# Kernel optimization log

Hardware: AMD Instinct MI355X
Metric: run time of the kernel (lower is better)

The kernel has to match this reference:

```python
import jax, jax.numpy as jnp
import numpy as np

B, S, D, H, DK = 32, 1024, 256, 8, 32
MASK_VALUE = -1e-30  # note: NOT -inf; masked scores become ~0 pre-softmax, faithful to source


def setup_inputs() -> dict:
    key = jax.random.key(0)
    ks = jax.random.split(key, 7)
    query = jax.random.normal(ks[0], (B, S, D), dtype=jnp.float32)
    key_t = jax.random.normal(ks[1], (B, S, D), dtype=jnp.float32)
    value = jax.random.normal(ks[2], (B, S, D), dtype=jnp.float32)
    # binary observation mask over key positions
    mask = (jax.random.uniform(ks[3], (B, S)) > 0.5).astype(jnp.float32)
    glorot = jax.nn.initializers.glorot_uniform(in_axis=1, out_axis=2)
    Wq = glorot(ks[4], (H, D, DK), jnp.float32)
    Wk = glorot(ks[5], (H, D, DK), jnp.float32)
    Wv = glorot(ks[6], (H, D, DK), jnp.float32)
    return {"query": query, "key": key_t, "value": value, "mask": mask,
            "Wq": Wq, "Wk": Wk, "Wv": Wv}


def reference(query, key, value, mask, Wq, Wk, Wv):
    # per-head projections, vectorized over heads: [B,S,D] x [H,D,DK] -> [B,H,S,DK]
    q = jnp.einsum('bsd,hdk->bhsk', query, Wq)
    k = jnp.einsum('bsd,hdk->bhsk', key, Wk)
    v = jnp.einsum('bsd,hdk->bhsk', value, Wv)
    # raw scores (no 1/sqrt(dk) scaling in source): [B,H,Sq,Sk]
    A = jnp.einsum('bhqk,bhsk->bhqs', q, k)
    m = mask[:, None, None, :]  # [B,1,1,Sk]
    A = m * A + (1.0 - m) * MASK_VALUE  # multiplicative mask, NOT additive
    A = jax.nn.softmax(A, axis=-1)
    out = jnp.einsum('bhqs,bhsk->bhqk', A, v)  # [B,H,Sq,DK]
    # concat heads along last dim, matching torch.cat order
    return out.transpose(0, 2, 1, 3).reshape(B, S, H * DK)
```

## Files before the change

kernel.cpp:

```cpp
#include <hip/hip_runtime.h>
#include <math.h>

#define B_  32
#define S_  1024
#define D_  256
#define H_  8
#define DK_ 32
#define MASKV (-1e-30f)
#define LOG2E 1.44269504f

typedef __attribute__((ext_vector_type(4))) short bf4_t;
typedef __attribute__((ext_vector_type(8))) short bf8_t;
typedef __attribute__((ext_vector_type(4))) float f4_t;

__device__ __forceinline__ unsigned fbits(float x) {
    union { float f; unsigned u; } v; v.f = x; return v.u;
}
__device__ __forceinline__ float bitsf(unsigned u) {
    union { unsigned u; float f; } v; v.u = u; return v.f;
}

#if __has_builtin(__builtin_amdgcn_exp2f)
#define EXP2F(x) __builtin_amdgcn_exp2f(x)
#else
#define EXP2F(x) __expf((x) * 0.69314718f)
#endif

__device__ __forceinline__ void gld16(const void* g, void* l) {
    __builtin_amdgcn_global_load_lds(
        (const __attribute__((address_space(1))) void*)g,
        (__attribute__((address_space(3))) void*)l, 16, 0, 0);
}

#define PSEL 0x07060302u


__global__ __launch_bounds__(256) void prep_w(
    const float* __restrict__ Wq, const float* __restrict__ Wk,
    const float* __restrict__ Wv, short* __restrict__ WpH, short* __restrict__ WpL)
{
    const int a = blockIdx.x >> 3;
    const int h = blockIdx.x & 7;
    const float* W = (a == 0 ? Wq : (a == 1 ? Wk : Wv)) + (size_t)h * 256 * 32;
    const int t = threadIdx.x;
    const int k    = t & 31;
    const int dgrp = t >> 5;
    const int ng   = h * 2 + (k >> 4);
    const int l15  = k & 15;
#pragma unroll
    for (int jj = blockIdx.y * 2; jj < blockIdx.y * 2 + 2; ++jj) {
        const int d0 = jj * 32 + dgrp * 4;
        float x[4];
#pragma unroll
        for (int r = 0; r < 4; ++r) x[r] = W[(size_t)(d0 + r) * 32 + k];
        unsigned hu[4], lu[4];
#pragma unroll
        for (int r = 0; r < 4; ++r) {
            unsigned hb = (fbits(x[r]) + 0x8000u) & 0xFFFF0000u;
            hu[r] = hb;
            lu[r] = fbits(x[r] - bitsf(hb)) + 0x8000u;
        }
        uint2 hp = make_uint2(__builtin_amdgcn_perm(hu[1], hu[0], PSEL),
                              __builtin_amdgcn_perm(hu[3], hu[2], PSEL));
        uint2 lp = make_uint2(__builtin_amdgcn_perm(lu[1], lu[0], PSEL),
                              __builtin_amdgcn_perm(lu[3], lu[2], PSEL));
        const int quad = (d0 >> 3) & 3;
        const int jb   = d0 & 7;
        size_t off = (size_t)a * 65536
                   + ((size_t)(jj * 16 + ng) * 64 + quad * 16 + l15) * 8 + jb;
        *(uint2*)&WpH[off] = hp;
        *(uint2*)&WpL[off] = lp;
    }
}

__global__ __launch_bounds__(256) void proj_kernel(
    const float* __restrict__ Xq, const float* __restrict__ Xk,
    const float* __restrict__ Xv, const float* __restrict__ mask,
    const short* __restrict__ WpH, const short* __restrict__ WpL,
    short* __restrict__ qpH, short* __restrict__ qpL,
    short* __restrict__ kpH, short* __restrict__ kpL,
    short* __restrict__ vpT)
{
    __shared__ __align__(16) short XsH[8192];
    __shared__ __align__(16) short XsL[8192];

    const int a  = blockIdx.y;
    const float* X = (a == 0 ? Xq : (a == 1 ? Xk : Xv));
    const short* WH = WpH + (size_t)a * 65536;
    const short* WL = WpL + (size_t)a * 65536;
    const int m0 = blockIdx.x * 64;

    const int tid  = threadIdx.x;
    const int lane = tid & 63;
    const int wv   = tid >> 6;
    const int l15  = lane & 15;
    const int quad = lane >> 4;

    f4_t acc[4][4];
#pragma unroll
    for (int i = 0; i < 4; ++i)
#pragma unroll
        for (int j = 0; j < 4; ++j) acc[i][j] = (f4_t){0.f, 0.f, 0.f, 0.f};

    const int r    = tid >> 2;
    const int dseg = tid & 3;
    const int tix  = r >> 4;
    const int rl15 = r & 15;

    const short* WHb = WH + (wv * 4) * 512 + lane * 8;
    const short* WLb = WL + (wv * 4) * 512 + lane * 8;

    bf8_t wAh[4], wAl[4], wBh[4], wBl[4];

#define WLOAD(BUFh, BUFl, KC)                                                  \
    _Pragma("unroll")                                                          \
    for (int ns = 0; ns < 4; ++ns) {                                           \
        BUFh[ns] = *(const bf8_t*)&WHb[(KC) * 8192 + ns * 512];                \
        BUFl[ns] = *(const bf8_t*)&WLb[(KC) * 8192 + ns * 512];                \
    }

#define STAGE_X(H2)                                                            \
    {                                                                          \
        const float* xp = X + (size_t)(m0 + r) * 256 + (H2) * 128 + dseg * 32; \
        _Pragma("unroll")                                                      \
        for (int q = 0; q < 4; ++q) {                                          \
            float4 x0 = *(const float4*)(xp + q * 8);                          \
            float4 x1 = *(const float4*)(xp + q * 8 + 4);                      \
            float xv[8] = {x0.x, x0.y, x0.z, x0.w, x1.x, x1.y, x1.z, x1.w};    \
            bf8_t hi, lo;                                                      \
            _Pragma("unroll")                                                  \
            for (int j = 0; j < 8; ++j) {                                      \
                unsigned hu = (fbits(xv[j]) + 0x8000u) & 0xFFFF0000u;          \
                hi[j] = (short)(hu >> 16);                                     \
                lo[j] = (short)((fbits(xv[j] - bitsf(hu)) + 0x8000u) >> 16);   \
            }                                                                  \
            const int off = ((dseg * 4 + tix) * 64 + q * 16 + rl15) * 8;       \
            *(bf8_t*)&XsH[off] = hi;                                           \
            *(bf8_t*)&XsL[off] = lo;                                           \
        }                                                                      \
    }

#define COMPUTE(KCL, BUFh, BUFl)                                               \
    {                                                                          \
        bf8_t xH[4], xL[4];                                                    \
        _Pragma("unroll")                                                      \
        for (int t = 0; t < 4; ++t) {                                          \
            xH[t] = *(const bf8_t*)&XsH[(((KCL) * 4 + t) * 64 + lane) * 8];    \
            xL[t] = *(const bf8_t*)&XsL[(((KCL) * 4 + t) * 64 + lane) * 8];    \
        }                                                                      \
        _Pragma("unroll")                                                      \
        for (int ns = 0; ns < 4; ++ns) {                                       \
            _Pragma("unroll")                                                  \
            for (int t = 0; t < 4; ++t) {                                      \
                f4_t c = acc[t][ns];                                           \
                if (a < 2) {                                                   \
                    c = __builtin_amdgcn_mfma_f32_16x16x32_bf16(BUFh[ns], xH[t], c, 0, 0, 0); \
                    c = __builtin_amdgcn_mfma_f32_16x16x32_bf16(BUFl[ns], xH[t], c, 0, 0, 0); \
                    c = __builtin_amdgcn_mfma_f32_16x16x32_bf16(BUFh[ns], xL[t], c, 0, 0, 0); \
                } else {                                                       \
                    c = __builtin_amdgcn_mfma_f32_16x16x32_bf16(xH[t], BUFh[ns], c, 0, 0, 0); \
                    c = __builtin_amdgcn_mfma_f32_16x16x32_bf16(xH[t], BUFl[ns], c, 0, 0, 0); \
                    c = __builtin_amdgcn_mfma_f32_16x16x32_bf16(xL[t], BUFh[ns], c, 0, 0, 0); \
                }                                                              \
                acc[t][ns] = c;                                                \
            }                                                                  \
        }                                                                      \
    }

    WLOAD(wAh, wAl, 0)
    STAGE_X(0)
    __syncthreads();

    WLOAD(wBh, wBl, 1)  COMPUTE(0, wAh, wAl)
    WLOAD(wAh, wAl, 2)  COMPUTE(1, wBh, wBl)
    WLOAD(wBh, wBl, 3)  COMPUTE(2, wAh, wAl)
    WLOAD(wAh, wAl, 4)  COMPUTE(3, wBh, wBl)

    __syncthreads();
    STAGE_X(1)
    __syncthreads();

    WLOAD(wBh, wBl, 5)  COMPUTE(0, wAh, wAl)
    WLOAD(wAh, wAl, 6)  COMPUTE(1, wBh, wBl)
    WLOAD(wBh, wBl, 7)  COMPUTE(2, wAh, wAl)
                        COMPUTE(3, wBh, wBl)

#undef WLOAD
#undef STAGE_X
#undef COMPUTE

    const int b  = m0 >> 10;
    const int sB = m0 & 1023;
    if (a < 2) {
        short* dH = (a == 0) ? qpH : kpH;
        short* dL = (a == 0) ? qpL : kpL;
        const float* mbp = mask + (size_t)b * 1024;
#pragma unroll
        for (int t = 0; t < 4; ++t) {
            const int s = sB + t * 16 + l15;
            const float scale = (a == 0) ? LOG2E : mbp[s];
            const int grp = (sB >> 4) + t;
#pragma unroll
            for (int ns = 0; ns < 4; ++ns) {
                const int h_    = wv * 2 + (ns >> 1);
                const int quadA = (ns & 1) * 2 + (quad >> 1);
                const int jb    = (quad & 1) * 4;
                unsigned hu[4], lu[4];
#pragma unroll
                for (int rr = 0; rr < 4; ++rr) {
                    float x = acc[t][ns][rr] * scale;
                    unsigned h32 = fbits(x) + 0x8000u;
                    hu[rr] = h32;
                    float hf = bitsf(h32 & 0xFFFF0000u);
                    lu[rr] = fbits(x - hf) + 0x8000u;
                }
                uint2 hp = make_uint2(__builtin_amdgcn_perm(hu[1], hu[0], PSEL),
                                      __builtin_amdgcn_perm(hu[3], hu[2], PSEL));
                uint2 lp = make_uint2(__builtin_amdgcn_perm(lu[1], lu[0], PSEL),
                                      __builtin_amdgcn_perm(lu[3], lu[2], PSEL));
                size_t off = (((size_t)(b * 8 + h_) * 64 + grp) * 64
                              + quadA * 16 + l15) * 8 + jb;
                *(uint2*)&dH[off] = hp;
                *(uint2*)&dL[off] = lp;
            }
        }
    } else {
#pragma unroll
        for (int t = 0; t < 4; ++t) {
            int sr = sB + t * 16 + quad * 4;
#pragma unroll
            for (int ns = 0; ns < 4; ++ns) {
                int n = wv * 64 + ns * 16 + l15;
                int h = n >> 5, k = n & 31;
                unsigned eu[4];
#pragma unroll
                for (int rr = 0; rr < 4; ++rr) eu[rr] = fbits(acc[t][ns][rr]) + 0x8000u;
                uint2 pk = make_uint2(__builtin_amdgcn_perm(eu[1], eu[0], PSEL),
                                      __builtin_amdgcn_perm(eu[3], eu[2], PSEL));
                *(uint2*)&vpT[((size_t)(b * 8 + h) * 32 + k) * 1024 + sr] = pk;
            }
        }
    }
}

__global__ __launch_bounds__(256) void attn_kernel(
    const short* __restrict__ qpH, const short* __restrict__ qpL,
    const short* __restrict__ kpH, const short* __restrict__ kpL,
    const short* __restrict__ vpT, float* __restrict__ out)
{
    __shared__ __align__(16) short KsH[2][2048];
    __shared__ __align__(16) short KsL[2][2048];
    __shared__ __align__(16) short VsT[2][32 * 72];

    const int tid  = threadIdx.x;
    const int lane = tid & 63;
    const int wv   = tid >> 6;
    const int l15  = lane & 15;
    const int quad = lane >> 4;

    const int L  = (blockIdx.z * gridDim.y + blockIdx.y) * gridDim.x + blockIdx.x;
    const int li = L >> 3;
    const int bh = (L & 7) * 32 + (li >> 3);
    const int qt = li & 7;
    const int b  = bh >> 3;
    const int h  = bh & 7;
    const int woff = qt * 128 + wv * 32;

    bf8_t qh[2], ql[2];
#pragma unroll
    for (int qs = 0; qs < 2; ++qs) {
        const int grp = qt * 8 + wv * 2 + qs;
        size_t off = (((size_t)bh * 64 + grp) * 64 + lane) * 8;
        qh[qs] = *(const bf8_t*)&qpH[off];
        ql[qs] = *(const bf8_t*)&qpL[off];
    }

    f4_t accO[2][2];
    f4_t accS[2];
#pragma unroll
    for (int i = 0; i < 2; ++i) {
        accS[i] = (f4_t){0.f, 0.f, 0.f, 0.f};
#pragma unroll
        for (int j = 0; j < 2; ++j) accO[i][j] = (f4_t){0.f, 0.f, 0.f, 0.f};
    }
    const bf4_t ones4 = {(short)0x3F80, (short)0x3F80, (short)0x3F80, (short)0x3F80};

    const int dv = tid >> 3, seg = tid & 7;

    bf4_t vA[8], vB[8];
    bf4_t pfA[2][4], pfB[2][4];

#define TILE(KT, CUR, DO_STAGE, DO_PV, VIN, VOUT, PIN, POUT)                    \
    {                                                                           \
                      \
        _Pragma("unroll")                                                       \
        for (int ks = 0; ks < 4; ++ks) {                                        \
            VOUT[ks * 2]     = *(const bf4_t*)&VsT[CUR][l15 * 72 + ks * 16 + quad * 4];       \
            VOUT[ks * 2 + 1] = *(const bf4_t*)&VsT[CUR][(16 + l15) * 72 + ks * 16 + quad * 4];\
        }                                                                       \
                    \
        uint4 vreg;                                                             \
        if (DO_STAGE) {                                                         \
            size_t toff = ((size_t)bh * 64 + (size_t)((KT) + 1) * 4) * 512;     \
            gld16(kpH + toff + wv * 512 + lane * 8, (char*)KsH[(CUR) ^ 1] + wv * 1024); \
            gld16(kpL + toff + wv * 512 + lane * 8, (char*)KsL[(CUR) ^ 1] + wv * 1024); \
            vreg = *(const uint4*)&vpT[((size_t)bh * 32 + dv) * 1024            \
                                       + (size_t)((KT) + 1) * 64 + seg * 8];    \
        }                                                                       \
        __builtin_amdgcn_s_setprio(1);                                          \
                       \
        _Pragma("unroll")                                                       \
        for (int ks = 0; ks < 4; ++ks) {                                        \
            bf8_t kh = *(const bf8_t*)&KsH[CUR][ks * 512 + lane * 8];           \
            bf8_t kl = *(const bf8_t*)&KsL[CUR][ks * 512 + lane * 8];           \
            f4_t sc[2];                                                         \
            _Pragma("unroll")                                                   \
            for (int qs = 0; qs < 2; ++qs) {                                    \
                f4_t c = __builtin_amdgcn_mfma_f32_16x16x32_bf16(kh, qh[qs],    \
                             (f4_t){0.f, 0.f, 0.f, 0.f}, 0, 0, 0);              \
                c = __builtin_amdgcn_mfma_f32_16x16x32_bf16(kl, qh[qs], c, 0, 0, 0); \
                c = __builtin_amdgcn_mfma_f32_16x16x32_bf16(kh, ql[qs], c, 0, 0, 0); \
                sc[qs] = c;                                                     \
            }                                                                   \
            if (DO_PV) {                                                        \
                _Pragma("unroll")                                               \
                for (int qs = 0; qs < 2; ++qs) {                                \
                    accO[qs][0] = __builtin_amdgcn_mfma_f32_16x16x16bf16_1k(    \
                                      VIN[ks * 2], PIN[qs][ks], accO[qs][0], 0, 0, 0);     \
                    accO[qs][1] = __builtin_amdgcn_mfma_f32_16x16x16bf16_1k(    \
                                      VIN[ks * 2 + 1], PIN[qs][ks], accO[qs][1], 0, 0, 0); \
                    accS[qs]    = __builtin_amdgcn_mfma_f32_16x16x16bf16_1k(    \
                                      ones4, PIN[qs][ks], accS[qs], 0, 0, 0);   \
                }                                                               \
            }                                                                   \
            _Pragma("unroll")                                                   \
            for (int qs = 0; qs < 2; ++qs) {                                    \
                unsigned eu[4];                                                 \
                _Pragma("unroll")                                               \
                for (int r = 0; r < 4; ++r)                                     \
                    eu[r] = fbits(EXP2F(sc[qs][r]));      \
                union { uint2 u; bf4_t v; } cv;                                 \
                cv.u = make_uint2(__builtin_amdgcn_perm(eu[1], eu[0], PSEL),    \
                                  __builtin_amdgcn_perm(eu[3], eu[2], PSEL));   \
                POUT[qs][ks] = cv.v;                                            \
            }                                                                   \
        }                                                                       \
        __builtin_amdgcn_s_setprio(0);                                          \
                 \
        if (DO_STAGE) *(uint4*)&VsT[(CUR) ^ 1][dv * 72 + seg * 8] = vreg;       \
        __syncthreads();                                                        \
    }

    {
        size_t toff = ((size_t)bh * 64) * 512;
        gld16(kpH + toff + wv * 512 + lane * 8, (char*)KsH[0] + wv * 1024);
        gld16(kpL + toff + wv * 512 + lane * 8, (char*)KsL[0] + wv * 1024);
        uint4 v0 = *(const uint4*)&vpT[((size_t)bh * 32 + dv) * 1024 + seg * 8];
        *(uint4*)&VsT[0][dv * 72 + seg * 8] = v0;
    }
    __syncthreads();

    TILE(0, 0, 1, 0, vA, vA, pfA, pfA)
    for (int i = 0; i < 7; ++i) {
        TILE(2 * i + 1, 1, 1, 1, vA, vB, pfA, pfB)
        TILE(2 * i + 2, 0, 1, 1, vB, vA, pfB, pfA)
    }
    TILE(15, 1, 0, 1, vA, vB, pfA, pfB)

#pragma unroll
    for (int ks = 0; ks < 4; ++ks) {
#pragma unroll
        for (int qs = 0; qs < 2; ++qs) {
            accO[qs][0] = __builtin_amdgcn_mfma_f32_16x16x16bf16_1k(
                              vB[ks * 2], pfB[qs][ks], accO[qs][0], 0, 0, 0);
            accO[qs][1] = __builtin_amdgcn_mfma_f32_16x16x16bf16_1k(
                              vB[ks * 2 + 1], pfB[qs][ks], accO[qs][1], 0, 0, 0);
            accS[qs]    = __builtin_amdgcn_mfma_f32_16x16x16bf16_1k(
                              ones4, pfB[qs][ks], accS[qs], 0, 0, 0);
        }
    }
#undef TILE

#pragma unroll
    for (int qs = 0; qs < 2; ++qs) {
        float inv = 1.0f / accS[qs][0];
        int s = woff + qs * 16 + l15;
        float* op = out + ((size_t)b * 1024 + s) * 256 + h * 32;
#pragma unroll
        for (int dvs = 0; dvs < 2; ++dvs) {
            float4 o4 = make_float4(accO[qs][dvs][0] * inv, accO[qs][dvs][1] * inv,
                                    accO[qs][dvs][2] * inv, accO[qs][dvs][3] * inv);
            *(float4*)&op[dvs * 16 + quad * 4] = o4;
        }
    }
}

extern "C" void kernel_launch(void* const* d_in, const int* in_sizes, int n_in,
                              void* d_out, int out_size, void* d_ws, size_t ws_size,
                              hipStream_t stream)
{
    const float* query = (const float*)d_in[0];
    const float* key   = (const float*)d_in[1];
    const float* value = (const float*)d_in[2];
    const float* mask  = (const float*)d_in[3];
    const float* Wq    = (const float*)d_in[4];
    const float* Wk    = (const float*)d_in[5];
    const float* Wv    = (const float*)d_in[6];
    float* out = (float*)d_out;

    const size_t per = (size_t)B_ * H_ * S_ * DK_;
    short* qpH = (short*)d_ws;
    short* qpL = qpH + per;
    short* kpH = qpL + per;
    short* kpL = kpH + per;
    short* vpT = kpL + per;
    short* WpH = vpT + per;
    short* WpL = WpH + 3 * 256 * 256;

    prep_w<<<dim3(24, 4), 256, 0, stream>>>(Wq, Wk, Wv, WpH, WpL);
    proj_kernel<<<dim3(512, 3), 256, 0, stream>>>(query, key, value, mask, WpH, WpL,
                                                  qpH, qpL, kpH, kpL, vpT);
    attn_kernel<<<dim3(8, H_, B_), 256, 0, stream>>>(qpH, qpL, kpH, kpL, vpT, out);
}
```

Before: 265.2 us.

## Load K and V fragments directly from global into registers, drop LDS staging

The attention kernel stops staging K and V tiles through shared memory with barriers. Each wave now loads its MFMA operand fragments straight from global memory into double-buffered registers. To make that possible, the projection kernel writes V in a new fragment-ready layout. This removes LDS traffic and the per-tile __syncthreads. In exchange, each of the four waves reads the same K/V data separately (relying on cache) and register pressure goes up.

```diff
diff --git a/kernel.cpp b/kernel.cpp
--- a/kernel.cpp
+++ b/kernel.cpp
@@ -25,12 +25,6 @@
 #else
 #define EXP2F(x) __expf((x) * 0.69314718f)
 #endif
-
-__device__ __forceinline__ void gld16(const void* g, void* l) {
-    __builtin_amdgcn_global_load_lds(
-        (const __attribute__((address_space(1))) void*)g,
-        (__attribute__((address_space(3))) void*)l, 16, 0, 0);
-}
 
 #define PSEL 0x07060302u
 
@@ -79,7 +73,7 @@
     const short* __restrict__ WpH, const short* __restrict__ WpL,
     short* __restrict__ qpH, short* __restrict__ qpL,
     short* __restrict__ kpH, short* __restrict__ kpL,
-    short* __restrict__ vpT)
+    short* __restrict__ vpF)
 {
     __shared__ __align__(16) short XsH[8192];
     __shared__ __align__(16) short XsL[8192];
@@ -225,19 +219,22 @@
             }
         }
     } else {
+        const int kt = sB >> 6;
 #pragma unroll
         for (int t = 0; t < 4; ++t) {
-            int sr = sB + t * 16 + quad * 4;
 #pragma unroll
             for (int ns = 0; ns < 4; ++ns) {
-                int n = wv * 64 + ns * 16 + l15;
-                int h = n >> 5, k = n & 31;
+                const int p  = ns & 1;
+                const int h_ = wv * 2 + (ns >> 1);
+                const int bh = b * 8 + h_;
                 unsigned eu[4];
 #pragma unroll
                 for (int rr = 0; rr < 4; ++rr) eu[rr] = fbits(acc[t][ns][rr]) + 0x8000u;
                 uint2 pk = make_uint2(__builtin_amdgcn_perm(eu[1], eu[0], PSEL),
                                       __builtin_amdgcn_perm(eu[3], eu[2], PSEL));
-                *(uint2*)&vpT[((size_t)(b * 8 + h) * 32 + k) * 1024 + sr] = pk;
+                size_t off = ((((size_t)bh * 16 + kt) * 4 + t) * 2 + p) * 256
+                           + (quad * 16 + l15) * 4;
+                *(uint2*)&vpF[off] = pk;
             }
         }
     }
@@ -246,12 +243,8 @@
 __global__ __launch_bounds__(256) void attn_kernel(
     const short* __restrict__ qpH, const short* __restrict__ qpL,
     const short* __restrict__ kpH, const short* __restrict__ kpL,
-    const short* __restrict__ vpT, float* __restrict__ out)
+    const short* __restrict__ vpF, float* __restrict__ out)
 {
-    __shared__ __align__(16) short KsH[2][2048];
-    __shared__ __align__(16) short KsL[2][2048];
-    __shared__ __align__(16) short VsT[2][32 * 72];
-
     const int tid  = threadIdx.x;
     const int lane = tid & 63;
     const int wv   = tid >> 6;
@@ -285,50 +278,49 @@
     }
     const bf4_t ones4 = {(short)0x3F80, (short)0x3F80, (short)0x3F80, (short)0x3F80};
 
-    const int dv = tid >> 3, seg = tid & 7;
-
-    bf4_t vA[8], vB[8];
+    const short* kHp = kpH + (size_t)bh * 64 * 512 + lane * 8;
+    const short* kLp = kpL + (size_t)bh * 64 * 512 + lane * 8;
+    const short* vFp = vpF + (size_t)bh * 32768 + lane * 4;
+
+    bf8_t kAh[4], kAl[4], kBh[4], kBl[4];
+    bf4_t vR[8];
     bf4_t pfA[2][4], pfB[2][4];
 
-#define TILE(KT, CUR, DO_STAGE, DO_PV, VIN, VOUT, PIN, POUT)                    \
+#define TILE(KCURh, KCURl, KNXTh, KNXTl, DO_KLOAD, DO_PV, PIN, POUT)            \
     {                                                                           \
-                      \
+        if (DO_KLOAD) {                                                         \
+            _Pragma("unroll")                                                   \
+            for (int ks = 0; ks < 4; ++ks) {                                    \
+                KNXTh[ks] = *(const bf8_t*)&kHp[ks * 512];                      \
+                KNXTl[ks] = *(const bf8_t*)&kLp[ks * 512];                      \
+            }                                                                   \
+        }                                                                       \
+        if (DO_PV) {                                                            \
+            _Pragma("unroll")                                                   \
+            for (int ks = 0; ks < 4; ++ks) {                                    \
+                vR[ks * 2]     = *(const bf4_t*)&vFp[(ks * 2) * 256];           \
+                vR[ks * 2 + 1] = *(const bf4_t*)&vFp[(ks * 2 + 1) * 256];       \
+            }                                                                   \
+        }                                                                       \
+        __builtin_amdgcn_s_setprio(1);                                          \
         _Pragma("unroll")                                                       \
         for (int ks = 0; ks < 4; ++ks) {                                        \
-            VOUT[ks * 2]     = *(const bf4_t*)&VsT[CUR][l15 * 72 + ks * 16 + quad * 4];       \
-            VOUT[ks * 2 + 1] = *(const bf4_t*)&VsT[CUR][(16 + l15) * 72 + ks * 16 + quad * 4];\
-        }                                                                       \
-                    \
-        uint4 vreg;                                                             \
-        if (DO_STAGE) {                                                         \
-            size_t toff = ((size_t)bh * 64 + (size_t)((KT) + 1) * 4) * 512;     \
-            gld16(kpH + toff + wv * 512 + lane * 8, (char*)KsH[(CUR) ^ 1] + wv * 1024); \
-            gld16(kpL + toff + wv * 512 + lane * 8, (char*)KsL[(CUR) ^ 1] + wv * 1024); \
-            vreg = *(const uint4*)&vpT[((size_t)bh * 32 + dv) * 1024            \
-                                       + (size_t)((KT) + 1) * 64 + seg * 8];    \
-        }                                                                       \
-        __builtin_amdgcn_s_setprio(1);                                          \
-                       \
-        _Pragma("unroll")                                                       \
-        for (int ks = 0; ks < 4; ++ks) {                                        \
-            bf8_t kh = *(const bf8_t*)&KsH[CUR][ks * 512 + lane * 8];           \
-            bf8_t kl = *(const bf8_t*)&KsL[CUR][ks * 512 + lane * 8];           \
             f4_t sc[2];                                                         \
             _Pragma("unroll")                                                   \
             for (int qs = 0; qs < 2; ++qs) {                                    \
-                f4_t c = __builtin_amdgcn_mfma_f32_16x16x32_bf16(kh, qh[qs],    \
+                f4_t c = __builtin_amdgcn_mfma_f32_16x16x32_bf16(KCURh[ks], qh[qs], \
                              (f4_t){0.f, 0.f, 0.f, 0.f}, 0, 0, 0);              \
-                c = __builtin_amdgcn_mfma_f32_16x16x32_bf16(kl, qh[qs], c, 0, 0, 0); \
-                c = __builtin_amdgcn_mfma_f32_16x16x32_bf16(kh, ql[qs], c, 0, 0, 0); \
+                c = __builtin_amdgcn_mfma_f32_16x16x32_bf16(KCURl[ks], qh[qs], c, 0, 0, 0); \
+                c = __builtin_amdgcn_mfma_f32_16x16x32_bf16(KCURh[ks], ql[qs], c, 0, 0, 0); \
                 sc[qs] = c;                                                     \
             }                                                                   \
             if (DO_PV) {                                                        \
                 _Pragma("unroll")                                               \
                 for (int qs = 0; qs < 2; ++qs) {                                \
                     accO[qs][0] = __builtin_amdgcn_mfma_f32_16x16x16bf16_1k(    \
-                                      VIN[ks * 2], PIN[qs][ks], accO[qs][0], 0, 0, 0);     \
+                                      vR[ks * 2], PIN[qs][ks], accO[qs][0], 0, 0, 0);     \
                     accO[qs][1] = __builtin_amdgcn_mfma_f32_16x16x16bf16_1k(    \
-                                      VIN[ks * 2 + 1], PIN[qs][ks], accO[qs][1], 0, 0, 0); \
+                                      vR[ks * 2 + 1], PIN[qs][ks], accO[qs][1], 0, 0, 0); \
                     accS[qs]    = __builtin_amdgcn_mfma_f32_16x16x16bf16_1k(    \
                                       ones4, PIN[qs][ks], accS[qs], 0, 0, 0);   \
                 }                                                               \
@@ -346,35 +338,40 @@
             }                                                                   \
         }                                                                       \
         __builtin_amdgcn_s_setprio(0);                                          \
-                 \
-        if (DO_STAGE) *(uint4*)&VsT[(CUR) ^ 1][dv * 72 + seg * 8] = vreg;       \
-        __syncthreads();                                                        \
-    }
-
-    {
-        size_t toff = ((size_t)bh * 64) * 512;
-        gld16(kpH + toff + wv * 512 + lane * 8, (char*)KsH[0] + wv * 1024);
-        gld16(kpL + toff + wv * 512 + lane * 8, (char*)KsL[0] + wv * 1024);
-        uint4 v0 = *(const uint4*)&vpT[((size_t)bh * 32 + dv) * 1024 + seg * 8];
-        *(uint4*)&VsT[0][dv * 72 + seg * 8] = v0;
-    }
-    __syncthreads();
-
-    TILE(0, 0, 1, 0, vA, vA, pfA, pfA)
+    }
+
+#pragma unroll
+    for (int ks = 0; ks < 4; ++ks) {
+        kAh[ks] = *(const bf8_t*)&kHp[ks * 512];
+        kAl[ks] = *(const bf8_t*)&kLp[ks * 512];
+    }
+    kHp += 2048; kLp += 2048;
+
+    TILE(kAh, kAl, kBh, kBl, 1, 0, pfA, pfA)
+    kHp += 2048; kLp += 2048;
+
     for (int i = 0; i < 7; ++i) {
-        TILE(2 * i + 1, 1, 1, 1, vA, vB, pfA, pfB)
-        TILE(2 * i + 2, 0, 1, 1, vB, vA, pfB, pfA)
-    }
-    TILE(15, 1, 0, 1, vA, vB, pfA, pfB)
-
+        TILE(kBh, kBl, kAh, kAl, 1, 1, pfA, pfB)
+        kHp += 2048; kLp += 2048; vFp += 2048;
+        TILE(kAh, kAl, kBh, kBl, 1, 1, pfB, pfA)
+        kHp += 2048; kLp += 2048; vFp += 2048;
+    }
+    TILE(kBh, kBl, kAh, kAl, 0, 1, pfA, pfB)
+    vFp += 2048;
+
+#pragma unroll
+    for (int ks = 0; ks < 4; ++ks) {
+        vR[ks * 2]     = *(const bf4_t*)&vFp[(ks * 2) * 256];
+        vR[ks * 2 + 1] = *(const bf4_t*)&vFp[(ks * 2 + 1) * 256];
+    }
 #pragma unroll
     for (int ks = 0; ks < 4; ++ks) {
 #pragma unroll
         for (int qs = 0; qs < 2; ++qs) {
             accO[qs][0] = __builtin_amdgcn_mfma_f32_16x16x16bf16_1k(
-                              vB[ks * 2], pfB[qs][ks], accO[qs][0], 0, 0, 0);
+                              vR[ks * 2], pfB[qs][ks], accO[qs][0], 0, 0, 0);
             accO[qs][1] = __builtin_amdgcn_mfma_f32_16x16x16bf16_1k(
-                              vB[ks * 2 + 1], pfB[qs][ks], accO[qs][1], 0, 0, 0);
+                              vR[ks * 2 + 1], pfB[qs][ks], accO[qs][1], 0, 0, 0);
             accS[qs]    = __builtin_amdgcn_mfma_f32_16x16x16bf16_1k(
                               ones4, pfB[qs][ks], accS[qs], 0, 0, 0);
         }
@@ -413,12 +410,12 @@
     short* qpL = qpH + per;
     short* kpH = qpL + per;
     short* kpL = kpH + per;
-    short* vpT = kpL + per;
-    short* WpH = vpT + per;
+    short* vpF = kpL + per;
+    short* WpH = vpF + per;
     short* WpL = WpH + 3 * 256 * 256;
 
     prep_w<<<dim3(24, 4), 256, 0, stream>>>(Wq, Wk, Wv, WpH, WpL);
     proj_kernel<<<dim3(512, 3), 256, 0, stream>>>(query, key, value, mask, WpH, WpL,
-                                                  qpH, qpL, kpH, kpL, vpT);
-    attn_kernel<<<dim3(8, H_, B_), 256, 0, stream>>>(qpH, qpL, kpH, kpL, vpT, out);
-}
+                                                  qpH, qpL, kpH, kpL, vpF);
+    attn_kernel<<<dim3(8, H_, B_), 256, 0, stream>>>(qpH, qpL, kpH, kpL, vpF, out);
+}
```

Result: faster. 257.8 us (-2.8%).
